# Optimization experiments

Measured on AMD Instinct MI355X. Metric: run time of the kernel, lower is better.

## Reference

```python
import jax, jax.numpy as jnp
import numpy as np

D = 100  # input_size


def _gru_scan(x, h0, wi, wh, bi, bh):
    # x: [B,T,Din], h0: [B,H], wi: [3H,Din], wh: [3H,H]  (PyTorch r,z,n gate order)
    xw = jnp.einsum('btd,gd->btg', x, wi) + bi  # [B,T,3H]
    def step(h, xt):
        gh = h @ wh.T + bh
        xr, xz, xn = jnp.split(xt, 3, axis=-1)
        hr, hz, hn = jnp.split(gh, 3, axis=-1)
        r = jax.nn.sigmoid(xr + hr)
        z = jax.nn.sigmoid(xz + hz)
        n = jnp.tanh(xn + r * hn)
        hn2 = (1 - z) * n + z * h
        return hn2, hn2
    _, ys = jax.lax.scan(step, h0, jnp.swapaxes(xw, 0, 1))
    return jnp.swapaxes(ys, 0, 1)  # [B,T,H]


def _bigru(x, wi, wh, bi, bh):
    B = x.shape[0]
    H = wh.shape[-1]
    h0 = jnp.zeros((B, H), x.dtype)
    f = _gru_scan(x, h0, wi[0], wh[0], bi[0], bh[0])
    b = _gru_scan(x[:, ::-1], h0, wi[1], wh[1], bi[1], bh[1])[:, ::-1]
    return jnp.concatenate([f, b], axis=-1)


def _gru_cell(x, h, wi, wh, bi, bh):
    gx = x @ wi.T + bi
    gh = h @ wh.T + bh
    xr, xz, xn = jnp.split(gx, 3, axis=-1)
    hr, hz, hn = jnp.split(gh, 3, axis=-1)
    r = jax.nn.sigmoid(xr + hr)
    z = jax.nn.sigmoid(xz + hz)
    n = jnp.tanh(xn + r * hn)
    return (1 - z) * n + z * h


def setup_inputs() -> dict:
    key = jax.random.key(0)
    ks = iter(jax.random.split(key, 40))
    def n(shape, s=0.08):
        return (jax.random.normal(next(ks), shape) * s).astype(jnp.float32)
    B, T, L, V = 32, 512, 64, 400000
    inp = {
        'x_word': jax.random.randint(next(ks), (B, T), 0, V),
        'x_query': jax.random.randint(next(ks), (B, L), 0, V),
        'embed': n((V, D), 0.3),
        'ctx_wi': n((2, 3 * D, D)), 'ctx_wh': n((2, 3 * D, D)),
        'ctx_bi': n((2, 3 * D)), 'ctx_bh': n((2, 3 * D)),
        'mod0_wi': n((2, 3 * D, 8 * D)), 'mod0_wh': n((2, 3 * D, D)),
        'mod0_bi': n((2, 3 * D)), 'mod0_bh': n((2, 3 * D)),
        'mod1_wi': n((2, 3 * D, 2 * D)), 'mod1_wh': n((2, 3 * D, D)),
        'mod1_bi': n((2, 3 * D)), 'mod1_bh': n((2, 3 * D)),
        'w_sim': n((6 * D,)),
        'enc_wi': n((12 * D, 2 * D)), 'enc_wh': n((12 * D, 4 * D)),
        'enc_bi': n((12 * D,)), 'enc_bh': n((12 * D,)),
        'dec_wi': n((12 * D, 2 * D)), 'dec_wh': n((12 * D, 4 * D)),
        'dec_bi': n((12 * D,)), 'dec_bh': n((12 * D,)),
        'w1': n((2 * D, 4 * D)), 'w2': n((2 * D, 4 * D)), 'vt': n((2 * D,)),
    }
    return inp


def reference(x_word, x_query, embed, ctx_wi, ctx_wh, ctx_bi, ctx_bh,
              mod0_wi, mod0_wh, mod0_bi, mod0_bh, mod1_wi, mod1_wh, mod1_bi, mod1_bh,
              w_sim, enc_wi, enc_wh, enc_bi, enc_bh, dec_wi, dec_wh, dec_bi, dec_bh,
              w1, w2, vt):
    B, T = x_word.shape
    # shared bidirectional context encoder over both context and query
    h = _bigru(embed[x_word], ctx_wi, ctx_wh, ctx_bi, ctx_bh)   # [B,T,2D]
    u = _bigru(embed[x_query], ctx_wi, ctx_wh, ctx_bi, ctx_bh)  # [B,L,2D]
    # trilinear similarity W @ cat(h,u,h*u), fused (no [B,T,L,6D] materialization)
    w1s, w2s, w3s = jnp.split(w_sim, 3)
    S = (jnp.einsum('btd,d->bt', h, w1s)[:, :, None]
         + jnp.einsum('bld,d->bl', u, w2s)[:, None, :]
         + jnp.einsum('btd,bld->btl', h * w3s, u))               # [B,T,L]
    c2q = jnp.einsum('btl,bld->btd', jax.nn.softmax(S, axis=-1), u)
    b_att = jax.nn.softmax(jnp.max(S, axis=2), axis=-1)          # [B,T]
    q2c = jnp.einsum('bt,btd->bd', b_att, h)[:, None, :]         # [B,1,2D]
    G = jnp.concatenate([h, c2q, h * c2q, h * q2c], axis=-1)     # [B,T,8D]
    # 2-layer bidirectional modeling GRU
    M = _bigru(G, mod0_wi, mod0_wh, mod0_bi, mod0_bh)
    M = _bigru(M, mod1_wi, mod1_wh, mod1_bi, mod1_bh)            # [B,T,2D]
    # pointer network
    enc = _gru_scan(M, jnp.zeros((B, 4 * D), M.dtype), enc_wi, enc_wh, enc_bi, enc_bh)  # [B,T,4D]
    enc_w1 = jnp.einsum('bth,ph->btp', enc, w1)                  # precompute W1 @ enc
    hid = jnp.zeros((B, 4 * D), M.dtype)
    dec_in = jnp.zeros((B, 2 * D), M.dtype)  # never updated (as in original)
    probs = []
    for _ in range(2):  # answers = 2 (start, end)
        hid = _gru_cell(dec_in, hid, dec_wi, dec_wh, dec_bi, dec_bh)
        blend = jnp.tanh(enc_w1 + (hid @ w2.T)[:, None, :])      # [B,T,2D]
        out = jnp.einsum('btp,p->bt', blend, vt)
        probs.append(jax.nn.log_softmax(out, axis=-1))
    return jnp.stack(probs, axis=1)  # [B,2,T]
```

## Files before the change

### kernel.cpp

```cpp
#include <hip/hip_runtime.h>
#include <hip/hip_bf16.h>

typedef __hip_bfloat16 bf16;
typedef unsigned long long u64;
typedef __attribute__((ext_vector_type(8))) short s8v;
typedef __attribute__((ext_vector_type(4))) short s4v;
typedef __attribute__((ext_vector_type(4))) float f4v;

#define DEV __device__ __forceinline__

DEV float to_f32(float x) { return x; }
DEV float to_f32(bf16 x) { return __bfloat162float(x); }
DEV void store_c(float* p, float v) { *p = v; }
DEV void store_c(bf16* p, float v) { *p = __float2bfloat16(v); }
DEV float sigmf(float x) { return 1.f / (1.f + __expf(-x)); }
DEV short f2bs(float x) { bf16 h = __float2bfloat16(x); return *(short*)&h; }

__global__ void cvt_all(const float* __restrict__ s0, bf16* __restrict__ d0,
                        const float* __restrict__ s1, bf16* __restrict__ d1,
                        const float* __restrict__ s2, bf16* __restrict__ d2,
                        const float* __restrict__ s3, bf16* __restrict__ d3,
                        const float* __restrict__ s4, bf16* __restrict__ d4) {
  int i = blockIdx.x * blockDim.x + threadIdx.x;
  if (i < 60000) d0[i] = __float2bfloat16(s0[i]);
  i -= 60000;
  if (i >= 0 && i < 480000) d1[i] = __float2bfloat16(s1[i]);
  i -= 480000;
  if (i >= 0 && i < 120000) d2[i] = __float2bfloat16(s2[i]);
  i -= 120000;
  if (i >= 0 && i < 240000) d3[i] = __float2bfloat16(s3[i]);
  i -= 240000;
  if (i >= 0 && i < 80000) d4[i] = __float2bfloat16(s4[i]);
}

template <typename TC, bool HAS_BIAS, bool GATHER>
__global__ __launch_bounds__(256) void gemm_mfma(
    const bf16* __restrict__ A, const int* __restrict__ idx,
    const float* __restrict__ embedp, const bf16* __restrict__ W,
    const float* __restrict__ bias, TC* __restrict__ C,
    int M, int N, int K) {
  __shared__ short Als[2][128 * 32];
  __shared__ short Wls[2][128 * 32];
  const int tid = threadIdx.x;
  const int m0 = blockIdx.x * 128;
  const int n0 = blockIdx.y * 128;
  const int lane = tid & 63;
  const int wv = tid >> 6;
  const int wm = wv >> 1, wn = wv & 1;
  const int lq = lane >> 4, lr = lane & 15;
  const int row2 = tid >> 1;
  const int half = tid & 1;

  int vrow = 0;
  if (GATHER) vrow = idx[m0 + row2];
  const int nrow = n0 + row2;

  s4v ra[4], rw[4];
  auto load_regs = [&](int k0) {
#pragma unroll
    for (int ss = 0; ss < 4; ++ss) {
      int kk = k0 + half * 16 + ss * 4;
      if (GATHER) {
        if (kk + 4 <= K) {
          float4 a4 = *(const float4*)(embedp + (size_t)vrow * 100 + kk);
          ra[ss] = (s4v){f2bs(a4.x), f2bs(a4.y), f2bs(a4.z), f2bs(a4.w)};
        } else {
          s4v v = {0, 0, 0, 0};
#pragma unroll
          for (int j = 0; j < 4; ++j)
            if (kk + j < K) v[j] = f2bs(embedp[(size_t)vrow * 100 + kk + j]);
          ra[ss] = v;
        }
      } else {
        const short* src = (const short*)(A + (size_t)(m0 + row2) * K + kk);
        if (kk + 4 <= K) {
          ra[ss] = *(const s4v*)src;
        } else {
          s4v v = {0, 0, 0, 0};
#pragma unroll
          for (int j = 0; j < 4; ++j)
            if (kk + j < K) v[j] = src[j];
          ra[ss] = v;
        }
      }
      if (nrow < N) {
        const short* src = (const short*)(W + (size_t)nrow * K + kk);
        if (kk + 4 <= K) {
          rw[ss] = *(const s4v*)src;
        } else {
          s4v v = {0, 0, 0, 0};
#pragma unroll
          for (int j = 0; j < 4; ++j)
            if (kk + j < K) v[j] = src[j];
          rw[ss] = v;
        }
      } else {
        rw[ss] = (s4v){0, 0, 0, 0};
      }
    }
  };
  auto write_lds = [&](int buf) {
#pragma unroll
    for (int ss = 0; ss < 4; ++ss) {
      *(s4v*)&Als[buf][row2 * 32 + half * 16 + ss * 4] = ra[ss];
      *(s4v*)&Wls[buf][row2 * 32 + half * 16 + ss * 4] = rw[ss];
    }
  };

  f4v acc[4][4];
#pragma unroll
  for (int i = 0; i < 4; ++i)
#pragma unroll
    for (int j = 0; j < 4; ++j) acc[i][j] = (f4v){0.f, 0.f, 0.f, 0.f};

  const int nk = (K + 31) / 32;
  load_regs(0);
  write_lds(0);
  __syncthreads();
  int cur = 0;
  for (int ki = 0; ki < nk; ++ki) {
    if (ki + 1 < nk) load_regs((ki + 1) * 32);
    s8v af[4], bfr[4];
#pragma unroll
    for (int mi = 0; mi < 4; ++mi) {
      int r = wm * 64 + mi * 16 + lr;
      af[mi] = *(const s8v*)&Als[cur][r * 32 + lq * 8];
    }
#pragma unroll
    for (int ni = 0; ni < 4; ++ni) {
      int r = wn * 64 + ni * 16 + lr;
      bfr[ni] = *(const s8v*)&Wls[cur][r * 32 + lq * 8];
    }
#pragma unroll
    for (int mi = 0; mi < 4; ++mi)
#pragma unroll
      for (int ni = 0; ni < 4; ++ni)
        acc[mi][ni] = __builtin_amdgcn_mfma_f32_16x16x32_bf16(af[mi], bfr[ni], acc[mi][ni], 0, 0, 0);
    if (ki + 1 < nk) write_lds(cur ^ 1);
    __syncthreads();
    cur ^= 1;
  }
#pragma unroll
  for (int mi = 0; mi < 4; ++mi) {
#pragma unroll
    for (int ni = 0; ni < 4; ++ni) {
      int n = n0 + wn * 64 + ni * 16 + lr;
      if (n >= N) continue;
      float bv = HAS_BIAS ? bias[n] : 0.f;
#pragma unroll
      for (int r = 0; r < 4; ++r) {
        int m = m0 + wm * 64 + mi * 16 + lq * 4 + r;
        store_c(&C[(size_t)m * N + n], acc[mi][ni][r] + bv);
      }
    }
  }
}

template <typename TO>
__global__ __launch_bounds__(256) void gru_scan100_1b(
    const bf16* __restrict__ xw0, const bf16* __restrict__ xw1,
    const float* __restrict__ wh,
    const float* __restrict__ bh,
    TO* __restrict__ out0, TO* __restrict__ out1,
    int T0, int T1) {
  const int b = blockIdx.x;
  const int y = blockIdx.y;
  const int which = y >> 1, dir = y & 1;
  const bf16* xw = which ? xw1 : xw0;
  TO* out = which ? out1 : out0;
  const int T = which ? T1 : T0;
  __shared__ float h_s[2][100];
  const int tid = threadIdx.x;
  const int i = tid >> 1, half = tid & 1;
  const bool act = (tid < 200);
  float wr[50], wz[50], wn[50];
  float br = 0.f, bz = 0.f, bn = 0.f;
  if (act) {
    const float* wb = wh + (size_t)dir * 30000;
    const float* rowr = wb + (size_t)i * 100 + half * 50;
    const float* rowz = wb + (size_t)(100 + i) * 100 + half * 50;
    const float* rown = wb + (size_t)(200 + i) * 100 + half * 50;
#pragma unroll
    for (int c = 0; c < 25; ++c) {
      float2 vr = *(const float2*)(rowr + 2 * c);
      wr[2 * c] = vr.x; wr[2 * c + 1] = vr.y;
      float2 vz = *(const float2*)(rowz + 2 * c);
      wz[2 * c] = vz.x; wz[2 * c + 1] = vz.y;
      float2 vn = *(const float2*)(rown + 2 * c);
      wn[2 * c] = vn.x; wn[2 * c + 1] = vn.y;
    }
    if (half == 0) {
      br = bh[dir * 300 + i];
      bz = bh[dir * 300 + 100 + i];
      bn = bh[dir * 300 + 200 + i];
    }
  }
  if (tid < 100) h_s[0][tid] = 0.f;
  float pxr = 0.f, pxz = 0.f, pxn = 0.f;
  if (act && half == 0) {
    int t0 = dir ? (T - 1) : 0;
    size_t base = ((size_t)b * T + t0) * 600 + dir * 300;
    pxr = to_f32(xw[base + i]);
    pxz = to_f32(xw[base + 100 + i]);
    pxn = to_f32(xw[base + 200 + i]);
  }
  __syncthreads();
  int cur = 0;
  for (int step = 0; step < T; ++step) {
    int t = dir ? (T - 1 - step) : step;
    if (act) {
      const float* hp = &h_s[cur][half * 50];
      float a0 = br, a1 = 0.f, z0 = bz, z1 = 0.f, n0 = bn, n1 = 0.f;
#pragma unroll
      for (int c = 0; c < 25; ++c) {
        float2 h2 = *(const float2*)(hp + 2 * c);
        a0 += wr[2 * c] * h2.x; a1 += wr[2 * c + 1] * h2.y;
        z0 += wz[2 * c] * h2.x; z1 += wz[2 * c + 1] * h2.y;
        n0 += wn[2 * c] * h2.x; n1 += wn[2 * c + 1] * h2.y;
      }
      float gr = a0 + a1, gz = z0 + z1, gn = n0 + n1;
      gr += __shfl_xor(gr, 1);
      gz += __shfl_xor(gz, 1);
      gn += __shfl_xor(gn, 1);
      if (half == 0) {
        float hprev = h_s[cur][i];
        float rr = sigmf(pxr + gr);
        float zz = sigmf(pxz + gz);
        float nn = tanhf(pxn + rr * gn);
        float hn = (1.f - zz) * nn + zz * hprev;
        h_s[cur ^ 1][i] = hn;
        store_c(&out[((size_t)b * T + t) * 200 + dir * 100 + i], hn);
        if (step + 1 < T) {
          int tn = dir ? (T - 2 - step) : (step + 1);
          size_t basen = ((size_t)b * T + tn) * 600 + dir * 300;
          pxr = to_f32(xw[basen + i]);
          pxz = to_f32(xw[basen + 100 + i]);
          pxn = to_f32(xw[basen + 200 + i]);
        }
      }
    }
    __syncthreads();
    cur ^= 1;
  }
}

__global__ __launch_bounds__(640) void gru_scan_enc_tag(
    const bf16* __restrict__ xw,
    const float* __restrict__ wh,
    const float* __restrict__ bh,
    bf16* __restrict__ out,
    u64* __restrict__ hx,
    int T) {
  const int b = blockIdx.x, s = blockIdx.y;
  __shared__ float h_s[400];
  __shared__ float g_s[150];
  const int tid = threadIdx.x;
  const int g = tid >> 2, p = tid & 3;
  const bool active = (tid < 600);
  float w[100];
  float bias = 0.f;
  if (active) {
    int i = g % 50, grp = g / 50;
    int gidx = grp * 400 + s * 50 + i;
    const float* wrow = wh + (size_t)gidx * 400 + p * 100;
#pragma unroll
    for (int c = 0; c < 25; ++c) {
      float4 v = *(const float4*)(wrow + 4 * c);
      w[4 * c] = v.x; w[4 * c + 1] = v.y; w[4 * c + 2] = v.z; w[4 * c + 3] = v.w;
    }
    if (p == 0) bias = bh[gidx];
  }
  for (int k = tid; k < 400; k += 640) h_s[k] = 0.f;
  const int myi = s * 50 + tid;
  float pxr = 0.f, pxz = 0.f, pxn = 0.f;
  if (tid < 50) {
    size_t base0 = (size_t)b * T * 1200;
    pxr = to_f32(xw[base0 + myi]);
    pxz = to_f32(xw[base0 + 400 + myi]);
    pxn = to_f32(xw[base0 + 800 + myi]);
  }
  __syncthreads();

  for (int t = 0; t < T; ++t) {
    if (active) {
      const int hb = p * 100;
      float4 hbuf[25];
#pragma unroll
      for (int c = 0; c < 25; ++c) hbuf[c] = *(const float4*)(&h_s[hb + 4 * c]);
      float a0 = bias, a1 = 0.f, a2 = 0.f, a3 = 0.f;
#pragma unroll
      for (int c = 0; c < 25; ++c) {
        a0 += w[4 * c] * hbuf[c].x; a1 += w[4 * c + 1] * hbuf[c].y;
        a2 += w[4 * c + 2] * hbuf[c].z; a3 += w[4 * c + 3] * hbuf[c].w;
      }
      float acc = (a0 + a1) + (a2 + a3);
      acc += __shfl_xor(acc, 1);
      acc += __shfl_xor(acc, 2);
      if (p == 0) g_s[g] = acc;
    }
    __syncthreads();
    const int par = (t + 1) & 1;
    u64* hxp = hx + ((size_t)b * 2 + par) * 400;
    if (tid < 50) {
      float rr = sigmf(pxr + g_s[tid]);
      float zz = sigmf(pxz + g_s[50 + tid]);
      float nn = tanhf(pxn + rr * g_s[100 + tid]);
      float hn = (1.f - zz) * nn + zz * h_s[myi];
      out[((size_t)b * T + t) * 400 + myi] = __float2bfloat16(hn);
      h_s[myi] = hn;
      u64 pack = (u64)__float_as_uint(hn) | ((u64)(unsigned)(t + 1) << 32);
      __hip_atomic_store(&hxp[myi], pack, __ATOMIC_RELAXED, __HIP_MEMORY_SCOPE_AGENT);
      if (t + 1 < T) {
        size_t basen = ((size_t)b * T + (t + 1)) * 1200;
        pxr = to_f32(xw[basen + myi]);
        pxz = to_f32(xw[basen + 400 + myi]);
        pxn = to_f32(xw[basen + 800 + myi]);
      }
    }
    if (tid < 400 && (tid / 50) != s) {
      const u64* src = &hxp[tid];
      u64 v;
      for (;;) {
        v = __hip_atomic_load(src, __ATOMIC_RELAXED, __HIP_MEMORY_SCOPE_AGENT);
        if ((unsigned)(v >> 32) == (unsigned)(t + 1)) break;
        __builtin_amdgcn_s_sleep(1);
      }
      h_s[tid] = __uint_as_float((unsigned)v);
    }
    __syncthreads();
  }
}

__global__ __launch_bounds__(256) void attn_main(
    const float* __restrict__ h, const float* __restrict__ u,
    const float* __restrict__ w_sim, float* __restrict__ c2q,
    float* __restrict__ smax, int T) {
  const int b = blockIdx.x;
  const int t0 = blockIdx.y * 32;
  __shared__ float u_s[64 * 201];
  __shared__ float w1_s[200], w2_s[200], w3_s[200];
  __shared__ float th_s[32], tu_s[64];
  __shared__ float hw3_s[200];
  __shared__ float Sp[4][64];
  __shared__ float A_s[64];
  const int tid = threadIdx.x;
  for (int i = tid; i < 64 * 200; i += 256) {
    int l = i / 200, d = i - l * 200;
    u_s[l * 201 + d] = u[((size_t)b * 64 + l) * 200 + d];
  }
  if (tid < 200) {
    w1_s[tid] = w_sim[tid];
    w2_s[tid] = w_sim[200 + tid];
    w3_s[tid] = w_sim[400 + tid];
  }
  __syncthreads();
  {
    int r = tid >> 2, sg = tid & 3;
    float p = 0.f;
    for (int j = 0; j < 50; ++j) p += u_s[r * 201 + sg * 50 + j] * w2_s[sg * 50 + j];
    p += __shfl_down(p, 2);
    p += __shfl_down(p, 1);
    if (sg == 0) tu_s[r] = p;
  }
  {
    int r = tid >> 3, sg = tid & 7;
    float p = 0.f;
    const float* hr = h + ((size_t)b * T + t0 + r) * 200 + sg * 25;
    for (int j = 0; j < 25; ++j) p += hr[j] * w1_s[sg * 25 + j];
    p += __shfl_down(p, 4);
    p += __shfl_down(p, 2);
    p += __shfl_down(p, 1);
    if (sg == 0) th_s[r] = p;
  }
  __syncthreads();
  for (int tt = 0; tt < 32; ++tt) {
    int t = t0 + tt;
    if (tid < 200) hw3_s[tid] = h[((size_t)b * T + t) * 200 + tid] * w3_s[tid];
    __syncthreads();
    int l = tid & 63, q = tid >> 6;
    float p = 0.f;
    for (int d = q * 50; d < q * 50 + 50; ++d) p += hw3_s[d] * u_s[l * 201 + d];
    Sp[q][l] = p;
    __syncthreads();
    if (tid < 64) {
      float s = th_s[tt] + tu_s[l] + Sp[0][l] + Sp[1][l] + Sp[2][l] + Sp[3][l];
      float m = s;
      for (int off = 32; off; off >>= 1) m = fmaxf(m, __shfl_xor(m, off));
      float e = __expf(s - m);
      float ssum = e;
      for (int off = 32; off; off >>= 1) ssum += __shfl_xor(ssum, off);
      A_s[l] = e / ssum;
      if (l == 0) smax[b * T + t] = m;
    }
    __syncthreads();
    if (tid < 200) {
      float acc = 0.f;
      for (int l2 = 0; l2 < 64; ++l2) acc += A_s[l2] * u_s[l2 * 201 + tid];
      c2q[((size_t)b * T + t) * 200 + tid] = acc;
    }
    __syncthreads();
  }
}

__global__ __launch_bounds__(256) void softmax_q2c(
    const float* __restrict__ smaxv, const float* __restrict__ h,
    float* __restrict__ q2c, int T) {
  int b = blockIdx.x;
  int tid = threadIdx.x;
  __shared__ float red[256];
  __shared__ float batt_s[512];
  float m = -1e30f;
  for (int t = tid; t < T; t += 256) m = fmaxf(m, smaxv[b * T + t]);
  red[tid] = m;
  __syncthreads();
  for (int s = 128; s; s >>= 1) {
    if (tid < s) red[tid] = fmaxf(red[tid], red[tid + s]);
    __syncthreads();
  }
  m = red[0];
  __syncthreads();
  float sum = 0.f;
  for (int t = tid; t < T; t += 256) {
    float e = __expf(smaxv[b * T + t] - m);
    batt_s[t] = e;
    sum += e;
  }
  red[tid] = sum;
  __syncthreads();
  for (int s = 128; s; s >>= 1) {
    if (tid < s) red[tid] += red[tid + s];
    __syncthreads();
  }
  float inv = 1.f / red[0];
  __syncthreads();
  if (tid < 200) {
    float acc = 0.f;
    for (int t = 0; t < T; ++t) acc += batt_s[t] * h[((size_t)b * T + t) * 200 + tid];
    q2c[b * 200 + tid] = acc * inv;
  }
}

__global__ void build_G(const float* __restrict__ h, const float* __restrict__ c2q,
                        const float* __restrict__ q2c, bf16* __restrict__ G, int T) {
  size_t i = (size_t)blockIdx.x * blockDim.x + threadIdx.x;
  if (i >= (size_t)32 * T * 200) return;
  size_t row = i / 200;
  int d = (int)(i - row * 200);
  int b = (int)(row / T);
  float hv = h[i];
  float cv = c2q[i];
  float qv = q2c[b * 200 + d];
  bf16* g = G + row * 800;
  g[d] = __float2bfloat16(hv);
  g[200 + d] = __float2bfloat16(cv);
  g[400 + d] = __float2bfloat16(hv * cv);
  g[600 + d] = __float2bfloat16(hv * qv);
}

__global__ __launch_bounds__(512) void decoder_small(
    const float* __restrict__ dwh, const float* __restrict__ dbi,
    const float* __restrict__ dbh, const float* __restrict__ w2,
    float* __restrict__ d2out) {
  __shared__ float hid[400];
  __shared__ float hid2[400];
  __shared__ float gh[1200];
  const int tid = threadIdx.x;
  if (tid < 400) {
    float r = sigmf(dbi[tid] + dbh[tid]);
    float z = sigmf(dbi[400 + tid] + dbh[400 + tid]);
    float n = tanhf(dbi[800 + tid] + r * dbh[800 + tid]);
    hid[tid] = (1.f - z) * n;
  }
  __syncthreads();
  if (tid < 200) {
    float a = 0.f;
    for (int k = 0; k < 400; ++k) a += w2[(size_t)tid * 400 + k] * hid[k];
    d2out[tid] = a;
  }
  for (int j = tid; j < 1200; j += 512) {
    float a = dbh[j];
    for (int k = 0; k < 400; ++k) a += dwh[(size_t)j * 400 + k] * hid[k];
    gh[j] = a;
  }
  __syncthreads();
  if (tid < 400) {
    float r = sigmf(dbi[tid] + gh[tid]);
    float z = sigmf(dbi[400 + tid] + gh[400 + tid]);
    float n = tanhf(dbi[800 + tid] + r * gh[800 + tid]);
    hid2[tid] = (1.f - z) * n + z * hid[tid];
  }
  __syncthreads();
  if (tid < 200) {
    float a = 0.f;
    for (int k = 0; k < 400; ++k) a += w2[(size_t)tid * 400 + k] * hid2[k];
    d2out[200 + tid] = a;
  }
}

__global__ __launch_bounds__(512) void logits_lsm(
    const float* __restrict__ encw1, const float* __restrict__ d2,
    const float* __restrict__ vt, float* __restrict__ outp, int T) {
  int b = blockIdx.x;
  __shared__ float lg[2][512];
  __shared__ float red[512];
  const int tid = threadIdx.x;
  const int wave = tid >> 6, lane = tid & 63;
  for (int r = wave; r < T; r += 8) {
    const float* e = encw1 + ((size_t)b * T + r) * 200;
    float s0 = 0.f, s1 = 0.f;
    for (int p = lane; p < 200; p += 64) {
      float ev = e[p], v = vt[p];
      s0 += tanhf(ev + d2[p]) * v;
      s1 += tanhf(ev + d2[200 + p]) * v;
    }
    for (int off = 32; off; off >>= 1) {
      s0 += __shfl_down(s0, off);
      s1 += __shfl_down(s1, off);
    }
    if (lane == 0) { lg[0][r] = s0; lg[1][r] = s1; }
  }
  __syncthreads();
  for (int it = 0; it < 2; ++it) {
    red[tid] = lg[it][tid];
    __syncthreads();
    for (int s = 256; s; s >>= 1) {
      if (tid < s) red[tid] = fmaxf(red[tid], red[tid + s]);
      __syncthreads();
    }
    float m = red[0];
    __syncthreads();
    red[tid] = __expf(lg[it][tid] - m);
    __syncthreads();
    for (int s = 256; s; s >>= 1) {
      if (tid < s) red[tid] += red[tid + s];
      __syncthreads();
    }
    float lse = m + __logf(red[0]);
    __syncthreads();
    outp[((size_t)b * 2 + it) * T + tid] = lg[it][tid] - lse;
  }
}

extern "C" void kernel_launch(void* const* d_in, const int* in_sizes, int n_in,
                              void* d_out, int out_size, void* d_ws, size_t ws_size,
                              hipStream_t stream) {
  (void)in_sizes; (void)n_in; (void)out_size; (void)ws_size;
  const int B = 32, T = 512, L = 64;
  const int BT = B * T;
  const int BL = B * L;

  const int* x_word = (const int*)d_in[0];
  const int* x_query = (const int*)d_in[1];
  const float* embed = (const float*)d_in[2];
  const float* ctx_wi = (const float*)d_in[3];
  const float* ctx_wh = (const float*)d_in[4];
  const float* ctx_bi = (const float*)d_in[5];
  const float* ctx_bh = (const float*)d_in[6];
  const float* mod0_wi = (const float*)d_in[7];
  const float* mod0_wh = (const float*)d_in[8];
  const float* mod0_bi = (const float*)d_in[9];
  const float* mod0_bh = (const float*)d_in[10];
  const float* mod1_wi = (const float*)d_in[11];
  const float* mod1_wh = (const float*)d_in[12];
  const float* mod1_bi = (const float*)d_in[13];
  const float* mod1_bh = (const float*)d_in[14];
  const float* w_sim = (const float*)d_in[15];
  const float* enc_wi = (const float*)d_in[16];
  const float* enc_wh = (const float*)d_in[17];
  const float* enc_bi = (const float*)d_in[18];
  const float* enc_bh = (const float*)d_in[19];
  const float* dec_wh = (const float*)d_in[21];
  const float* dec_bi = (const float*)d_in[22];
  const float* dec_bh = (const float*)d_in[23];
  const float* w1 = (const float*)d_in[24];
  const float* w2 = (const float*)d_in[25];
  const float* vt = (const float*)d_in[26];
  float* out_f = (float*)d_out;

  char* ws = (char*)d_ws;
  size_t off = 0;
  auto alloc = [&](size_t bytes) -> void* {
    void* p = ws + off;
    off += (bytes + 255) & ~(size_t)255;
    return p;
  };
  u64* hx = (u64*)alloc((size_t)B * 2 * 400 * 8);
  bf16* ctx_wibf = (bf16*)alloc((size_t)60000 * 2);
  bf16* mod0_wibf = (bf16*)alloc((size_t)480000 * 2);
  bf16* mod1_wibf = (bf16*)alloc((size_t)120000 * 2);
  bf16* enc_wibf = (bf16*)alloc((size_t)240000 * 2);
  bf16* w1bf = (bf16*)alloc((size_t)80000 * 2);
  char* RA = (char*)alloc((size_t)BT * 1200 * 2);
  bf16* xwFB = (bf16*)RA;
  bf16* xwe = (bf16*)RA;
  bf16* xwq = (bf16*)alloc((size_t)BL * 600 * 2);
  char* RB = (char*)alloc((size_t)BT * 800 * 2);
  bf16* G = (bf16*)RB;
  bf16* enc_outbf = (bf16*)RB;
  char* RC = (char*)alloc((size_t)2 * BT * 200 * 4);
  float* h_cat = (float*)RC;
  float* c2q = (float*)(RC + (size_t)BT * 200 * 4);
  bf16* M0bf = (bf16*)c2q;
  bf16* Mxbf = (bf16*)h_cat;
  float* encw1 = c2q;
  float* u_cat = (float*)alloc((size_t)BL * 200 * 4);
  float* smaxb = (float*)alloc((size_t)BT * 4);
  float* q2cb = (float*)alloc((size_t)B * 200 * 4);
  float* d2 = (float*)alloc((size_t)400 * 4);

  hipMemsetAsync(hx, 0, (size_t)B * 2 * 400 * 8, stream);

  cvt_all<<<(980000 + 255) / 256, 256, 0, stream>>>(ctx_wi, ctx_wibf, mod0_wi, mod0_wibf,
                                                    mod1_wi, mod1_wibf, enc_wi, enc_wibf,
                                                    w1, w1bf);

  gemm_mfma<bf16, true, true><<<dim3(BT / 128, 5), 256, 0, stream>>>(
      nullptr, x_word, embed, ctx_wibf, ctx_bi, xwFB, BT, 600, 100);
  gemm_mfma<bf16, true, true><<<dim3(BL / 128, 5), 256, 0, stream>>>(
      nullptr, x_query, embed, ctx_wibf, ctx_bi, xwq, BL, 600, 100);

  gru_scan100_1b<float><<<dim3(B, 4), 256, 0, stream>>>(
      xwFB, xwq, ctx_wh, ctx_bh, h_cat, u_cat, T, L);

  attn_main<<<dim3(B, T / 32), 256, 0, stream>>>(h_cat, u_cat, w_sim, c2q, smaxb, T);
  softmax_q2c<<<B, 256, 0, stream>>>(smaxb, h_cat, q2cb, T);
  build_G<<<(BT * 200 + 255) / 256, 256, 0, stream>>>(h_cat, c2q, q2cb, G, T);

  gemm_mfma<bf16, true, false><<<dim3(BT / 128, 5), 256, 0, stream>>>(
      G, nullptr, nullptr, mod0_wibf, mod0_bi, xwFB, BT, 600, 800);
  gru_scan100_1b<bf16><<<dim3(B, 2), 256, 0, stream>>>(
      xwFB, nullptr, mod0_wh, mod0_bh, M0bf, nullptr, T, T);

  gemm_mfma<bf16, true, false><<<dim3(BT / 128, 5), 256, 0, stream>>>(
      M0bf, nullptr, nullptr, mod1_wibf, mod1_bi, xwFB, BT, 600, 200);
  gru_scan100_1b<bf16><<<dim3(B, 2), 256, 0, stream>>>(
      xwFB, nullptr, mod1_wh, mod1_bh, Mxbf, nullptr, T, T);

  gemm_mfma<bf16, true, false><<<dim3(BT / 128, 10), 256, 0, stream>>>(
      Mxbf, nullptr, nullptr, enc_wibf, enc_bi, xwe, BT, 1200, 200);
  gru_scan_enc_tag<<<dim3(B, 8), 640, 0, stream>>>(xwe, enc_wh, enc_bh, enc_outbf, hx, T);
  gemm_mfma<float, false, false><<<dim3(BT / 128, 2), 256, 0, stream>>>(
      enc_outbf, nullptr, nullptr, w1bf, nullptr, encw1, BT, 200, 400);

  decoder_small<<<1, 512, 0, stream>>>(dec_wh, dec_bi, dec_bh, w2, d2);
  logits_lsm<<<B, 512, 0, stream>>>(encw1, d2, vt, out_f, T);
}
```

Before: 2.897 ms.

## Restructure encoder GRU scan to one barrier per step with double-buffered state

The encoder GRU scan now assigns each hidden unit's r, z and n gate rows to an 8-lane group, so every thread computes all three gate partial dot products and reduces them with shuffles. The gate shared-memory buffer and one of the two barriers per timestep are removed, and the hidden state is double-buffered. This cuts per-step synchronisation on the serial recurrence. In exchange each thread holds 150 weight registers instead of 100, which may pressure occupancy or spill, and the block now has 448 threads.

```diff
diff --git a/kernel.cpp b/kernel.cpp
--- a/kernel.cpp
+++ b/kernel.cpp
@@ -244,7 +244,7 @@
   }
 }
 
-__global__ __launch_bounds__(640) void gru_scan_enc_tag(
+__global__ __launch_bounds__(448) void gru_scan_enc_1b(
     const bf16* __restrict__ xw,
     const float* __restrict__ wh,
     const float* __restrict__ bh,
@@ -252,62 +252,66 @@
     u64* __restrict__ hx,
     int T) {
   const int b = blockIdx.x, s = blockIdx.y;
-  __shared__ float h_s[400];
-  __shared__ float g_s[150];
+  __shared__ float h_s[2][400];
   const int tid = threadIdx.x;
-  const int g = tid >> 2, p = tid & 3;
-  const bool active = (tid < 600);
-  float w[100];
-  float bias = 0.f;
-  if (active) {
-    int i = g % 50, grp = g / 50;
-    int gidx = grp * 400 + s * 50 + i;
-    const float* wrow = wh + (size_t)gidx * 400 + p * 100;
+  const int e = tid >> 3, p = tid & 7;
+  const bool act = (tid < 400);
+  const int myi = s * 50 + e;
+  float wr[50], wz[50], wn[50];
+  float br = 0.f, bz = 0.f, bn = 0.f;
+  if (act) {
+    int rrow = s * 50 + e, zrow = 400 + s * 50 + e, nrow = 800 + s * 50 + e;
+    const float* pr = wh + (size_t)rrow * 400 + p * 50;
+    const float* pz = wh + (size_t)zrow * 400 + p * 50;
+    const float* pn = wh + (size_t)nrow * 400 + p * 50;
 #pragma unroll
     for (int c = 0; c < 25; ++c) {
-      float4 v = *(const float4*)(wrow + 4 * c);
-      w[4 * c] = v.x; w[4 * c + 1] = v.y; w[4 * c + 2] = v.z; w[4 * c + 3] = v.w;
-    }
-    if (p == 0) bias = bh[gidx];
-  }
-  for (int k = tid; k < 400; k += 640) h_s[k] = 0.f;
-  const int myi = s * 50 + tid;
+      float2 vr = *(const float2*)(pr + 2 * c);
+      wr[2 * c] = vr.x; wr[2 * c + 1] = vr.y;
+      float2 vz = *(const float2*)(pz + 2 * c);
+      wz[2 * c] = vz.x; wz[2 * c + 1] = vz.y;
+      float2 vn = *(const float2*)(pn + 2 * c);
+      wn[2 * c] = vn.x; wn[2 * c + 1] = vn.y;
+    }
+    if (p == 0) { br = bh[rrow]; bz = bh[zrow]; bn = bh[nrow]; }
+  }
+  for (int k = tid; k < 400; k += 448) h_s[0][k] = 0.f;
   float pxr = 0.f, pxz = 0.f, pxn = 0.f;
-  if (tid < 50) {
+  if (act && p == 0) {
     size_t base0 = (size_t)b * T * 1200;
     pxr = to_f32(xw[base0 + myi]);
     pxz = to_f32(xw[base0 + 400 + myi]);
     pxn = to_f32(xw[base0 + 800 + myi]);
   }
   __syncthreads();
-
+  int cur = 0;
   for (int t = 0; t < T; ++t) {
-    if (active) {
-      const int hb = p * 100;
-      float4 hbuf[25];
-#pragma unroll
-      for (int c = 0; c < 25; ++c) hbuf[c] = *(const float4*)(&h_s[hb + 4 * c]);
-      float a0 = bias, a1 = 0.f, a2 = 0.f, a3 = 0.f;
+    float gr = br, gz = bz, gn = bn;
+    if (act) {
+      const float* hp = &h_s[cur][p * 50];
+      float a0 = gr, a1 = 0.f, z0 = gz, z1 = 0.f, n0 = gn, n1 = 0.f;
 #pragma unroll
       for (int c = 0; c < 25; ++c) {
-        a0 += w[4 * c] * hbuf[c].x; a1 += w[4 * c + 1] * hbuf[c].y;
-        a2 += w[4 * c + 2] * hbuf[c].z; a3 += w[4 * c + 3] * hbuf[c].w;
-      }
-      float acc = (a0 + a1) + (a2 + a3);
-      acc += __shfl_xor(acc, 1);
-      acc += __shfl_xor(acc, 2);
-      if (p == 0) g_s[g] = acc;
-    }
-    __syncthreads();
+        float2 h2 = *(const float2*)(hp + 2 * c);
+        a0 += wr[2 * c] * h2.x; a1 += wr[2 * c + 1] * h2.y;
+        z0 += wz[2 * c] * h2.x; z1 += wz[2 * c + 1] * h2.y;
+        n0 += wn[2 * c] * h2.x; n1 += wn[2 * c + 1] * h2.y;
+      }
+      gr = a0 + a1; gz = z0 + z1; gn = n0 + n1;
+      gr += __shfl_xor(gr, 1); gr += __shfl_xor(gr, 2); gr += __shfl_xor(gr, 4);
+      gz += __shfl_xor(gz, 1); gz += __shfl_xor(gz, 2); gz += __shfl_xor(gz, 4);
+      gn += __shfl_xor(gn, 1); gn += __shfl_xor(gn, 2); gn += __shfl_xor(gn, 4);
+    }
     const int par = (t + 1) & 1;
     u64* hxp = hx + ((size_t)b * 2 + par) * 400;
-    if (tid < 50) {
-      float rr = sigmf(pxr + g_s[tid]);
-      float zz = sigmf(pxz + g_s[50 + tid]);
-      float nn = tanhf(pxn + rr * g_s[100 + tid]);
-      float hn = (1.f - zz) * nn + zz * h_s[myi];
+    if (act && p == 0) {
+      float hprev = h_s[cur][myi];
+      float rr = sigmf(pxr + gr);
+      float zz = sigmf(pxz + gz);
+      float nn = tanhf(pxn + rr * gn);
+      float hn = (1.f - zz) * nn + zz * hprev;
       out[((size_t)b * T + t) * 400 + myi] = __float2bfloat16(hn);
-      h_s[myi] = hn;
+      h_s[cur ^ 1][myi] = hn;
       u64 pack = (u64)__float_as_uint(hn) | ((u64)(unsigned)(t + 1) << 32);
       __hip_atomic_store(&hxp[myi], pack, __ATOMIC_RELAXED, __HIP_MEMORY_SCOPE_AGENT);
       if (t + 1 < T) {
@@ -325,9 +329,10 @@
         if ((unsigned)(v >> 32) == (unsigned)(t + 1)) break;
         __builtin_amdgcn_s_sleep(1);
       }
-      h_s[tid] = __uint_as_float((unsigned)v);
-    }
-    __syncthreads();
+      h_s[cur ^ 1][tid] = __uint_as_float((unsigned)v);
+    }
+    __syncthreads();
+    cur ^= 1;
   }
 }
 
@@ -638,7 +643,7 @@
 
   gemm_mfma<bf16, true, false><<<dim3(BT / 128, 10), 256, 0, stream>>>(
       Mxbf, nullptr, nullptr, enc_wibf, enc_bi, xwe, BT, 1200, 200);
-  gru_scan_enc_tag<<<dim3(B, 8), 640, 0, stream>>>(xwe, enc_wh, enc_bh, enc_outbf, hx, T);
+  gru_scan_enc_1b<<<dim3(B, 8), 448, 0, stream>>>(xwe, enc_wh, enc_bh, enc_outbf, hx, T);
   gemm_mfma<float, false, false><<<dim3(BT / 128, 2), 256, 0, stream>>>(
       enc_outbf, nullptr, nullptr, w1bf, nullptr, encw1, BT, 200, 400);
 
```

After: 2.874 ms. No clear change (-0.8%).
